# Optimization experiments

Hardware: AMD Instinct MI355X
Metric: run time of the kernel (lower is better)

Reference implementation:

```python
import jax, jax.numpy as jnp
import numpy as np

EMBED_DIM = 512
SMOOTH = 4.0        # args.lambda_softmax
LAMBDA_LSE = 6.0    # args.lambda_lse
LEAKY_SLOPE = 0.1
EPS = 1e-8


def setup_inputs() -> dict:
    key = jax.random.key(0)
    k1, k2, k3 = jax.random.split(key, 3)
    n_contract, n_region = 32, 256
    n_law, max_len = 32, 256
    contracts = jax.random.normal(k1, (n_contract, n_region, EMBED_DIM), jnp.float32)
    laws = jax.random.normal(k2, (n_law, max_len, EMBED_DIM), jnp.float32)
    law_lens = jax.random.randint(k3, (n_law,), 128, max_len + 1, jnp.int32)
    return {"contracts": contracts, "laws": laws, "law_lens": law_lens}


def reference(contracts, laws, law_lens):
    # contracts: [C, R, D], laws: [N, L, D], law_lens: [N]
    n_law, max_len, d = laws.shape
    # mask[n, l] = 1 if word l is within law n's true length
    mask = (jnp.arange(max_len)[None, :] < law_lens[:, None]).astype(contracts.dtype)

    # attn = law @ contract^T / sqrt(D): [N, C, L, R]
    attn = jnp.einsum('nld,crd->nclr', laws, contracts) / jnp.sqrt(jnp.float32(d))
    attn = jax.nn.leaky_relu(attn, LEAKY_SLOPE)
    # l2norm over region dim (per law-word row)
    attn = attn / (jnp.linalg.norm(attn, axis=-1, keepdims=True) + EPS)
    attn = jax.nn.softmax(attn, axis=-1) * SMOOTH
    # zero out contributions from padded law words (ragged lengths)
    attn = attn * mask[:, None, :, None]

    # weighted_law: [N, C, R, D]
    wlaw = jnp.einsum('nld,nclr->ncrd', laws, attn)

    # cosine similarity along D: [N, C, R]
    w12 = jnp.sum(contracts[None] * wlaw, axis=-1)
    w1 = jnp.linalg.norm(contracts, axis=-1)[None]          # [1, C, R]
    w2 = jnp.linalg.norm(wlaw, axis=-1)                      # [N, C, R]
    sim = w12 / jnp.maximum(w1 * w2, EPS)

    # LogSumExp aggregation over regions -> [N, C]
    row_sim = jnp.log(jnp.sum(jnp.exp(sim * LAMBDA_LSE), axis=-1)) / LAMBDA_LSE
    # concatenate per-law columns -> [C, N]
    return row_sim.T
```

## Files before the change

### kernel.cpp

```cpp
#include <hip/hip_runtime.h>
#include <hip/hip_bf16.h>

#define CN 32
#define RN 256
#define DN 512
#define NN 32
#define LN 256

#define STAGE_OFF 131072
#define SMEM_TOTAL 163840

typedef short v8s __attribute__((ext_vector_type(8)));
typedef float v4f __attribute__((ext_vector_type(4)));
typedef const __attribute__((address_space(1))) void* gas1_t;
typedef __attribute__((address_space(3))) void* las3_t;

__device__ __forceinline__ void gl2lds16(const void* g, void* l) {
  __builtin_amdgcn_global_load_lds((gas1_t)g, (las3_t)l, 16, 0, 0);
}

__device__ __forceinline__ unsigned short f2bf(float x) {
  unsigned int u = __float_as_uint(x);
  u = (u + 0x7fffu + ((u >> 16) & 1u)) >> 16;
  return (unsigned short)u;
}
__device__ __forceinline__ float bf2f(unsigned short h) {
  return __uint_as_float(((unsigned int)h) << 16);
}

__device__ __forceinline__ unsigned int pkbf(float a, float b) {
  __hip_bfloat162 h = __float22bfloat162_rn(make_float2(a, b));
  unsigned int u;
  __builtin_memcpy(&u, &h, sizeof(u));
  return u;
}

__device__ __forceinline__ const v8s* stgFrag(const unsigned short* buf, int r,
                                              int quad) {
  return (const v8s*)(buf + r * 32 + ((quad ^ ((r >> 1) & 3)) << 3));
}

__device__ __forceinline__ int satIdx(int r, int col) {
  return (r << 8) | ((((col >> 3) ^ (r & 7)) << 3) | (col & 7));
}

__device__ __forceinline__ v8s ldFrag64(const float* buf, int r, int cp) {
  const float* p = buf + r * 64 + (((cp + r) & 7) << 3);
  const float4 x0 = ((const float4*)p)[0];
  const float4 x1 = ((const float4*)p)[1];
  unsigned short h[8];
  h[0] = f2bf(x0.x); h[1] = f2bf(x0.y); h[2] = f2bf(x0.z); h[3] = f2bf(x0.w);
  h[4] = f2bf(x1.x); h[5] = f2bf(x1.y); h[6] = f2bf(x1.z); h[7] = f2bf(x1.w);
  return *(v8s*)h;
}

__global__ __launch_bounds__(512) void setup_kernel(
    const float* __restrict__ con, const float* __restrict__ laws,
    unsigned short* __restrict__ lawsB, unsigned short* __restrict__ conB,
    float* __restrict__ cnorm, unsigned short* __restrict__ G) {
  const int bid = blockIdx.x;
  const int t = threadIdx.x;
  if (bid < 256) {
    __shared__ float slice[256 * 64];
    const int n = bid >> 3;
    const int m0 = (bid & 7) << 5;
    const int lane = t & 63;
    const int w = t >> 6;
    const int quad = lane >> 4;
    const int l16 = lane & 15;
    const int rg = w >> 2;
    const int cg = w & 3;
    const float* lawN = laws + n * (LN * DN);

    v4f acc[4];
#pragma unroll
    for (int b = 0; b < 4; ++b) acc[b] = (v4f){0.f, 0.f, 0.f, 0.f};

    for (int ch = 0; ch < 8; ++ch) {
      const int dk = ch << 6;
      __syncthreads();
#pragma unroll
      for (int i = 0; i < 8; ++i) {
        const int s = i * 512 + t;
        const int row = s >> 4;
        const int p = s & 15;
        const int srcCol = ((((p >> 1) - row) & 7) << 3) + ((p & 1) << 2);
        gl2lds16(lawN + row * DN + dk + srcCol, (char*)slice + s * 16);
      }
      __syncthreads();
#pragma unroll
      for (int step = 0; step < 2; ++step) {
        const int cp = quad + (step << 2);
        v8s af = ldFrag64(slice, m0 + rg * 16 + l16, cp);
#pragma unroll
        for (int ct = 0; ct < 4; ++ct) {
          v8s bf = ldFrag64(slice, cg * 64 + ct * 16 + l16, cp);
          acc[ct] = __builtin_amdgcn_mfma_f32_16x16x32_bf16(af, bf, acc[ct], 0, 0, 0);
        }
      }
    }
    unsigned short* g = G + n * (LN * LN);
#pragma unroll
    for (int ct = 0; ct < 4; ++ct)
#pragma unroll
      for (int reg = 0; reg < 4; ++reg) {
        const int l = m0 + rg * 16 + quad * 4 + reg;
        g[l * LN + cg * 64 + ct * 16 + l16] = f2bf(acc[ct][reg]);
      }
  } else if (bid < 1280) {
    const int r = (bid - 256) * 8 + (t >> 6);
    const int lane = t & 63;
    const float4* src = (const float4*)(con + r * DN + lane * 8);
    float4 x0 = src[0], x1 = src[1];
    unsigned short h[8];
    h[0] = f2bf(x0.x); h[1] = f2bf(x0.y); h[2] = f2bf(x0.z); h[3] = f2bf(x0.w);
    h[4] = f2bf(x1.x); h[5] = f2bf(x1.y); h[6] = f2bf(x1.z); h[7] = f2bf(x1.w);
    *(v8s*)(conB + r * DN + lane * 8) = *(v8s*)h;
    float s = x0.x * x0.x + x0.y * x0.y + x0.z * x0.z + x0.w * x0.w +
              x1.x * x1.x + x1.y * x1.y + x1.z * x1.z + x1.w * x1.w;
#pragma unroll
    for (int m = 1; m < 64; m <<= 1) s += __shfl_xor(s, m, 64);
    if (lane == 0) cnorm[r] = sqrtf(s);
  } else {
    const int off = (bid - 1280) * 4096 + t * 8;
    const float4* src = (const float4*)(laws + off);
    float4 x0 = src[0], x1 = src[1];
    unsigned short h[8];
    h[0] = f2bf(x0.x); h[1] = f2bf(x0.y); h[2] = f2bf(x0.z); h[3] = f2bf(x0.w);
    h[4] = f2bf(x1.x); h[5] = f2bf(x1.y); h[6] = f2bf(x1.z); h[7] = f2bf(x1.w);
    *(v8s*)(lawsB + off) = *(v8s*)h;
  }
}

__global__ __launch_bounds__(512, 2) void main_kernel(
    const int* __restrict__ law_lens, const unsigned short* __restrict__ lawsB,
    const unsigned short* __restrict__ conB, const unsigned short* __restrict__ Gm,
    const float* __restrict__ cnorm, float* __restrict__ out) {
  extern __shared__ char smem[];
  unsigned short* sAt = (unsigned short*)smem;
  char* stage = smem + STAGE_OFF;

  const int bid = blockIdx.x;
  const int n = bid >> 5;
  const int c = bid & 31;
  const int t = threadIdx.x;
  const int lane = t & 63;
  const int w = t >> 6;
  const int quad = lane >> 4;
  const int l16 = lane & 15;
  const int sub = t & 3;
  const int rQ = t >> 2;
  const int subx = sub ^ ((rQ >> 1) & 3);
  const int len = law_lens[n];
  const int nCh = (len + 31) >> 5;
  const bool active = (w * 32) < len;

  const unsigned short* lawN = lawsB + n * (LN * DN);
  const unsigned short* conC = conB + c * (RN * DN);
  const unsigned short* Gn = Gm + n * (LN * LN);

  float w12p[16];
#pragma unroll
  for (int i = 0; i < 16; ++i) w12p[i] = 0.f;

  {
    const unsigned short* a0p = lawN + (w * 32 + l16) * DN + quad * 8;
    const unsigned short* a1p = a0p + 16 * DN;

    v4f acc[2][16];
#pragma unroll
    for (int a = 0; a < 2; ++a)
#pragma unroll
      for (int b = 0; b < 16; ++b) acc[a][b] = (v4f){0.f, 0.f, 0.f, 0.f};

#pragma unroll
    for (int i = 0; i < 2; ++i)
      gl2lds16(conC + (i * 128 + rQ) * DN + subx * 8,
               stage + i * 8192 + t * 16);

    for (int ch = 0; ch < 16; ++ch) {
      const int dk = ch << 5;
      __syncthreads();
      v8s af0 = *(const v8s*)(a0p + dk);
      v8s af1 = *(const v8s*)(a1p + dk);
      __builtin_amdgcn_sched_barrier(0);
      if (ch < 15) {
        char* dst = stage + ((ch + 1) & 1) * 16384;
#pragma unroll
        for (int i = 0; i < 2; ++i)
          gl2lds16(conC + (i * 128 + rQ) * DN + (dk + 32) + subx * 8,
                   dst + i * 8192 + t * 16);
      }
      __builtin_amdgcn_sched_barrier(0);
      if (active) {
        const unsigned short* cs =
            (const unsigned short*)(stage + (ch & 1) * 16384);
#pragma unroll
        for (int rt = 0; rt < 16; ++rt) {
          v8s bf = *stgFrag(cs, rt * 16 + l16, quad);
          acc[0][rt] = __builtin_amdgcn_mfma_f32_16x16x32_bf16(af0, bf, acc[0][rt], 0, 0, 0);
          acc[1][rt] = __builtin_amdgcn_mfma_f32_16x16x32_bf16(af1, bf, acc[1][rt], 0, 0, 0);
        }
      }
    }

    __syncthreads();

#pragma unroll
    for (int i = 0; i < 2; ++i)
      gl2lds16(Gn + (i * 128 + rQ) * LN + subx * 8, stage + i * 8192 + t * 16);

    if (active) {
#pragma unroll
      for (int tl = 0; tl < 2; ++tl) {
        unsigned int pk[16][2];
        float a0s[16];
#pragma unroll
        for (int reg = 0; reg < 4; ++reg) {
          const int lg = w * 32 + tl * 16 + quad * 4 + reg;
          float ss = 0.f;
#pragma unroll
          for (int rt = 0; rt < 16; ++rt) {
            const float v = acc[tl][rt][reg] * 0.04419417382415922f;
            const float lv = v > 0.f ? v : 0.1f * v;
            ss += lv * lv;
          }
#pragma unroll
          for (int m = 1; m < 16; m <<= 1) ss += __shfl_xor(ss, m, 64);
          const float inv = 1.f / (sqrtf(ss) + 1e-8f);
          float e[16];
          float den = 0.f;
#pragma unroll
          for (int rt = 0; rt < 16; ++rt) {
            const float v = acc[tl][rt][reg] * 0.04419417382415922f;
            const float lv = v > 0.f ? v : 0.1f * v;
            e[rt] = __expf(lv * inv);
            den += e[rt];
          }
#pragma unroll
          for (int m = 1; m < 16; m <<= 1) den += __shfl_xor(den, m, 64);
          const float sc = (lg < len) ? 4.f / den : 0.f;
#pragma unroll
          for (int rt = 0; rt < 16; ++rt) {
            const float v = acc[tl][rt][reg] * 0.04419417382415922f;
            const float a = e[rt] * sc;
            w12p[rt] += a * v;
            if (reg & 1)
              pk[rt][reg >> 1] = pkbf(a0s[rt], a);
            else
              a0s[rt] = a;
          }
        }
        const int lg0 = w * 32 + tl * 16 + quad * 4;
#pragma unroll
        for (int rt = 0; rt < 16; ++rt)
          *(uint2*)(sAt + satIdx(rt * 16 + l16, lg0)) = *(uint2*)pk[rt];
      }
    } else {
      uint2 z;
      z.x = 0u;
      z.y = 0u;
#pragma unroll
      for (int tl = 0; tl < 2; ++tl) {
        const int lg0 = w * 32 + tl * 16 + quad * 4;
#pragma unroll
        for (int rt = 0; rt < 16; ++rt)
          *(uint2*)(sAt + satIdx(rt * 16 + l16, lg0)) = z;
      }
    }
  }

#pragma unroll
  for (int rt = 0; rt < 16; ++rt) {
    w12p[rt] += __shfl_xor(w12p[rt], 16, 64);
    w12p[rt] += __shfl_xor(w12p[rt], 32, 64);
  }

  float nsv[2][4];
  {
    v4f acc[2][16];
#pragma unroll
    for (int a = 0; a < 2; ++a)
#pragma unroll
      for (int b = 0; b < 16; ++b) acc[a][b] = (v4f){0.f, 0.f, 0.f, 0.f};

    for (int ch = 0; ch < nCh; ++ch) {
      const int lk = ch << 5;
      __syncthreads();
      v8s af0 = *(const v8s*)(sAt + satIdx(w * 32 + l16, lk + quad * 8));
      v8s af1 = *(const v8s*)(sAt + satIdx(w * 32 + 16 + l16, lk + quad * 8));
      __builtin_amdgcn_sched_barrier(0);
      if (ch < nCh - 1) {
        char* dst = stage + ((ch + 1) & 1) * 16384;
#pragma unroll
        for (int i = 0; i < 2; ++i)
          gl2lds16(Gn + (i * 128 + rQ) * LN + (lk + 32) + subx * 8,
                   dst + i * 8192 + t * 16);
      }
      __builtin_amdgcn_sched_barrier(0);
      const unsigned short* gs =
          (const unsigned short*)(stage + (ch & 1) * 16384);
#pragma unroll
      for (int lt = 0; lt < 16; ++lt) {
        v8s bf = *stgFrag(gs, lt * 16 + l16, quad);
        acc[0][lt] = __builtin_amdgcn_mfma_f32_16x16x32_bf16(af0, bf, acc[0][lt], 0, 0, 0);
        acc[1][lt] = __builtin_amdgcn_mfma_f32_16x16x32_bf16(af1, bf, acc[1][lt], 0, 0, 0);
      }
    }
#pragma unroll
    for (int tl = 0; tl < 2; ++tl) {
#pragma unroll
      for (int reg = 0; reg < 4; ++reg) {
        const int r = w * 32 + tl * 16 + quad * 4 + reg;
        float s = 0.f;
#pragma unroll
        for (int lt = 0; lt < 16; ++lt)
          s += acc[tl][lt][reg] * bf2f(sAt[satIdx(r, lt * 16 + l16)]);
#pragma unroll
        for (int m = 1; m < 16; m <<= 1) s += __shfl_xor(s, m, 64);
        nsv[tl][reg] = s;
      }
    }
  }

  float* w12s = (float*)stage;
  float* nsqS = (float*)(stage + 8192);
  float* red = (float*)(stage + 9216);
  __syncthreads();
  if (l16 == 0) {
#pragma unroll
    for (int tl = 0; tl < 2; ++tl)
#pragma unroll
      for (int reg = 0; reg < 4; ++reg)
        nsqS[w * 32 + tl * 16 + quad * 4 + reg] = nsv[tl][reg];
  }
  if (lane < 16) {
#pragma unroll
    for (int rt = 0; rt < 16; ++rt) w12s[w * 256 + rt * 16 + lane] = w12p[rt];
  }
  __syncthreads();
  float p = 0.f;
  if (t < 256) {
    float w12 = 0.f;
#pragma unroll
    for (int i = 0; i < 8; ++i) w12 += w12s[i * 256 + t];
    const float w1 = cnorm[c * RN + t];
    const float w2 = sqrtf(fmaxf(nsqS[t], 0.f));
    const float sim = (w12 * 22.627416997969522f) / fmaxf(w1 * w2, 1e-8f);
    p = __expf(6.f * sim);
  }
#pragma unroll
  for (int m = 1; m < 64; m <<= 1) p += __shfl_xor(p, m, 64);
  if (lane == 0) red[w] = p;
  __syncthreads();
  if (t == 0) {
    float s = 0.f;
#pragma unroll
    for (int i = 0; i < 8; ++i) s += red[i];
    out[c * NN + n] = logf(s) / 6.f;
  }
}

extern "C" void kernel_launch(void* const* d_in, const int* in_sizes, int n_in,
                              void* d_out, int out_size, void* d_ws, size_t ws_size,
                              hipStream_t stream) {
  (void)in_sizes; (void)n_in; (void)out_size;
  const float* contracts = (const float*)d_in[0];
  const float* laws = (const float*)d_in[1];
  const int* law_lens = (const int*)d_in[2];
  float* out = (float*)d_out;

  unsigned short* lawsB = (unsigned short*)d_ws;
  unsigned short* conB = lawsB + NN * LN * DN;
  unsigned short* G = conB + CN * RN * DN;
  float* cnorm = (float*)(G + NN * LN * LN);
  if (ws_size < (size_t)21004288) return;

  hipFuncSetAttribute((const void*)main_kernel,
                      hipFuncAttributeMaxDynamicSharedMemorySize, SMEM_TOTAL);

  setup_kernel<<<2304, 512, 0, stream>>>(contracts, laws, lawsB, conB, cnorm,
                                         G);
  main_kernel<<<1024, 512, SMEM_TOTAL, stream>>>(law_lens, lawsB, conB, G,
                                                 cnorm, out);
}
```

Measured before the change: 244.5 us.

## Merge setup work into 256 blocks with double-buffered Gram tiles; skip padded tiles

The setup kernel used three block roles: Gram-matrix blocks, contract conversion blocks and law conversion blocks. It now runs as a uniform grid of 256 blocks. Each block converts its share of laws and contracts to bf16 while the first Gram slice streams into LDS, and later slices are double-buffered through 128KB of dynamic shared memory. Separately, the main kernel skips MFMA column tiles and norm terms beyond the law's true length, cutting compute on padded words. Risks: fewer blocks means less parallelism, and the large LDS footprint limits occupancy in the setup kernel.

```diff
diff --git a/kernel.cpp b/kernel.cpp
--- a/kernel.cpp
+++ b/kernel.cpp
@@ -58,58 +58,41 @@
     const float* __restrict__ con, const float* __restrict__ laws,
     unsigned short* __restrict__ lawsB, unsigned short* __restrict__ conB,
     float* __restrict__ cnorm, unsigned short* __restrict__ G) {
+  extern __shared__ float slice[];
   const int bid = blockIdx.x;
   const int t = threadIdx.x;
-  if (bid < 256) {
-    __shared__ float slice[256 * 64];
-    const int n = bid >> 3;
-    const int m0 = (bid & 7) << 5;
-    const int lane = t & 63;
-    const int w = t >> 6;
-    const int quad = lane >> 4;
-    const int l16 = lane & 15;
-    const int rg = w >> 2;
-    const int cg = w & 3;
-    const float* lawN = laws + n * (LN * DN);
-
-    v4f acc[4];
-#pragma unroll
-    for (int b = 0; b < 4; ++b) acc[b] = (v4f){0.f, 0.f, 0.f, 0.f};
-
-    for (int ch = 0; ch < 8; ++ch) {
-      const int dk = ch << 6;
-      __syncthreads();
-#pragma unroll
-      for (int i = 0; i < 8; ++i) {
-        const int s = i * 512 + t;
-        const int row = s >> 4;
-        const int p = s & 15;
-        const int srcCol = ((((p >> 1) - row) & 7) << 3) + ((p & 1) << 2);
-        gl2lds16(lawN + row * DN + dk + srcCol, (char*)slice + s * 16);
-      }
-      __syncthreads();
-#pragma unroll
-      for (int step = 0; step < 2; ++step) {
-        const int cp = quad + (step << 2);
-        v8s af = ldFrag64(slice, m0 + rg * 16 + l16, cp);
-#pragma unroll
-        for (int ct = 0; ct < 4; ++ct) {
-          v8s bf = ldFrag64(slice, cg * 64 + ct * 16 + l16, cp);
-          acc[ct] = __builtin_amdgcn_mfma_f32_16x16x32_bf16(af, bf, acc[ct], 0, 0, 0);
-        }
-      }
-    }
-    unsigned short* g = G + n * (LN * LN);
-#pragma unroll
-    for (int ct = 0; ct < 4; ++ct)
-#pragma unroll
-      for (int reg = 0; reg < 4; ++reg) {
-        const int l = m0 + rg * 16 + quad * 4 + reg;
-        g[l * LN + cg * 64 + ct * 16 + l16] = f2bf(acc[ct][reg]);
-      }
-  } else if (bid < 1280) {
-    const int r = (bid - 256) * 8 + (t >> 6);
-    const int lane = t & 63;
+  const int n = bid >> 3;
+  const int m0 = (bid & 7) << 5;
+  const int lane = t & 63;
+  const int w = t >> 6;
+  const int quad = lane >> 4;
+  const int l16 = lane & 15;
+  const int rg = w >> 2;
+  const int cg = w & 3;
+  const float* lawN = laws + n * (LN * DN);
+
+#pragma unroll
+  for (int i = 0; i < 8; ++i) {
+    const int s = i * 512 + t;
+    const int row = s >> 4;
+    const int p = s & 15;
+    const int srcCol = ((((p >> 1) - row) & 7) << 3) + ((p & 1) << 2);
+    gl2lds16(lawN + row * DN + srcCol, (char*)slice + s * 16);
+  }
+
+#pragma unroll
+  for (int p = 0; p < 4; ++p) {
+    const int off = bid * 16384 + p * 4096 + t * 8;
+    const float4* src = (const float4*)(laws + off);
+    float4 x0 = src[0], x1 = src[1];
+    unsigned short h[8];
+    h[0] = f2bf(x0.x); h[1] = f2bf(x0.y); h[2] = f2bf(x0.z); h[3] = f2bf(x0.w);
+    h[4] = f2bf(x1.x); h[5] = f2bf(x1.y); h[6] = f2bf(x1.z); h[7] = f2bf(x1.w);
+    *(v8s*)(lawsB + off) = *(v8s*)h;
+  }
+#pragma unroll
+  for (int p = 0; p < 4; ++p) {
+    const int r = bid * 32 + p * 8 + w;
     const float4* src = (const float4*)(con + r * DN + lane * 8);
     float4 x0 = src[0], x1 = src[1];
     unsigned short h[8];
@@ -121,15 +104,46 @@
 #pragma unroll
     for (int m = 1; m < 64; m <<= 1) s += __shfl_xor(s, m, 64);
     if (lane == 0) cnorm[r] = sqrtf(s);
-  } else {
-    const int off = (bid - 1280) * 4096 + t * 8;
-    const float4* src = (const float4*)(laws + off);
-    float4 x0 = src[0], x1 = src[1];
-    unsigned short h[8];
-    h[0] = f2bf(x0.x); h[1] = f2bf(x0.y); h[2] = f2bf(x0.z); h[3] = f2bf(x0.w);
-    h[4] = f2bf(x1.x); h[5] = f2bf(x1.y); h[6] = f2bf(x1.z); h[7] = f2bf(x1.w);
-    *(v8s*)(lawsB + off) = *(v8s*)h;
-  }
+  }
+
+  v4f acc[4];
+#pragma unroll
+  for (int b = 0; b < 4; ++b) acc[b] = (v4f){0.f, 0.f, 0.f, 0.f};
+
+  for (int ch = 0; ch < 8; ++ch) {
+    __syncthreads();
+    if (ch < 7) {
+      const int dk = (ch + 1) << 6;
+      char* dst = (char*)slice + ((ch + 1) & 1) * 65536;
+#pragma unroll
+      for (int i = 0; i < 8; ++i) {
+        const int s = i * 512 + t;
+        const int row = s >> 4;
+        const int p = s & 15;
+        const int srcCol = ((((p >> 1) - row) & 7) << 3) + ((p & 1) << 2);
+        gl2lds16(lawN + row * DN + dk + srcCol, dst + s * 16);
+      }
+    }
+    const float* buf = slice + (ch & 1) * 16384;
+#pragma unroll
+    for (int step = 0; step < 2; ++step) {
+      const int cp = quad + (step << 2);
+      v8s af = ldFrag64(buf, m0 + rg * 16 + l16, cp);
+#pragma unroll
+      for (int ct = 0; ct < 4; ++ct) {
+        v8s bf = ldFrag64(buf, cg * 64 + ct * 16 + l16, cp);
+        acc[ct] = __builtin_amdgcn_mfma_f32_16x16x32_bf16(af, bf, acc[ct], 0, 0, 0);
+      }
+    }
+  }
+  unsigned short* g = G + n * (LN * LN);
+#pragma unroll
+  for (int ct = 0; ct < 4; ++ct)
+#pragma unroll
+    for (int reg = 0; reg < 4; ++reg) {
+      const int l = m0 + rg * 16 + quad * 4 + reg;
+      g[l * LN + cg * 64 + ct * 16 + l16] = f2bf(acc[ct][reg]);
+    }
 }
 
 __global__ __launch_bounds__(512, 2) void main_kernel(
@@ -153,6 +167,7 @@
   const int subx = sub ^ ((rQ >> 1) & 3);
   const int len = law_lens[n];
   const int nCh = (len + 31) >> 5;
+  const int nLt = (len + 15) >> 4;
   const bool active = (w * 32) < len;
 
   const unsigned short* lawN = lawsB + n * (LN * DN);
@@ -302,9 +317,11 @@
           (const unsigned short*)(stage + (ch & 1) * 16384);
 #pragma unroll
       for (int lt = 0; lt < 16; ++lt) {
-        v8s bf = *stgFrag(gs, lt * 16 + l16, quad);
-        acc[0][lt] = __builtin_amdgcn_mfma_f32_16x16x32_bf16(af0, bf, acc[0][lt], 0, 0, 0);
-        acc[1][lt] = __builtin_amdgcn_mfma_f32_16x16x32_bf16(af1, bf, acc[1][lt], 0, 0, 0);
+        if (lt < nLt) {
+          v8s bf = *stgFrag(gs, lt * 16 + l16, quad);
+          acc[0][lt] = __builtin_amdgcn_mfma_f32_16x16x32_bf16(af0, bf, acc[0][lt], 0, 0, 0);
+          acc[1][lt] = __builtin_amdgcn_mfma_f32_16x16x32_bf16(af1, bf, acc[1][lt], 0, 0, 0);
+        }
       }
     }
 #pragma unroll
@@ -314,8 +331,10 @@
         const int r = w * 32 + tl * 16 + quad * 4 + reg;
         float s = 0.f;
 #pragma unroll
-        for (int lt = 0; lt < 16; ++lt)
-          s += acc[tl][lt][reg] * bf2f(sAt[satIdx(r, lt * 16 + l16)]);
+        for (int lt = 0; lt < 16; ++lt) {
+          if (lt < nLt)
+            s += acc[tl][lt][reg] * bf2f(sAt[satIdx(r, lt * 16 + l16)]);
+        }
 #pragma unroll
         for (int m = 1; m < 16; m <<= 1) s += __shfl_xor(s, m, 64);
         nsv[tl][reg] = s;
@@ -376,11 +395,13 @@
   float* cnorm = (float*)(G + NN * LN * LN);
   if (ws_size < (size_t)21004288) return;
 
+  hipFuncSetAttribute((const void*)setup_kernel,
+                      hipFuncAttributeMaxDynamicSharedMemorySize, 131072);
   hipFuncSetAttribute((const void*)main_kernel,
                       hipFuncAttributeMaxDynamicSharedMemorySize, SMEM_TOTAL);
 
-  setup_kernel<<<2304, 512, 0, stream>>>(contracts, laws, lawsB, conB, cnorm,
-                                         G);
+  setup_kernel<<<256, 512, 131072, stream>>>(contracts, laws, lawsB, conB,
+                                             cnorm, G);
   main_kernel<<<1024, 512, SMEM_TOTAL, stream>>>(law_lens, lawsB, conB, G,
                                                  cnorm, out);
 }
```

Result: slower. 264.9 us (+8.3%).
